# Performance work log

Measured on AMD Instinct MI355X. Metric: run time of the kernel, lower is better.

## Reference

```python
import jax, jax.numpy as jnp
import numpy as np

B, L, D, H, DK, DV = 16, 512, 1024, 16, 64, 64
EPS = 1e-3  # LayerNormalization eps (added to sigma, not variance)


def _xavier(key, shape):
    fan_in, fan_out = shape[-2], shape[-1]
    std = float(np.sqrt(2.0 / (fan_in + fan_out)))
    return jax.random.normal(key, shape, jnp.float32) * std


def setup_inputs() -> dict:
    key = jax.random.key(0)
    ks = jax.random.split(key, 8)
    q = jax.random.normal(ks[0], (B, L, D), jnp.float32)
    k = jax.random.normal(ks[1], (B, L, D), jnp.float32)
    v = jax.random.normal(ks[2], (B, L, D), jnp.float32)
    # key-padding mask: last 64 key positions masked (True => -inf)
    key_pad = jnp.arange(L) >= (L - 64)
    attn_mask = jnp.broadcast_to(key_pad[None, None, :], (B, L, L))
    w_qs = _xavier(ks[3], (H, D, DK))
    w_ks = _xavier(ks[4], (H, D, DK))
    w_vs = _xavier(ks[5], (H, D, DV))
    proj_w = _xavier(ks[6], (H * DV, D))  # stored as (in, out)
    proj_b = jnp.zeros((D,), jnp.float32)
    ln_a = jnp.ones((D,), jnp.float32)
    ln_b = jnp.zeros((D,), jnp.float32)
    return {"q": q, "k": k, "v": v, "attn_mask": attn_mask,
            "w_qs": w_qs, "w_ks": w_ks, "w_vs": w_vs,
            "proj_w": proj_w, "proj_b": proj_b, "ln_a": ln_a, "ln_b": ln_b}


def reference(q, k, v, attn_mask, w_qs, w_ks, w_vs, proj_w, proj_b, ln_a, ln_b):
    n_head, d_model = w_qs.shape[0], q.shape[-1]
    mb, len_q = q.shape[0], q.shape[1]
    temper = jnp.sqrt(jnp.asarray(d_model, q.dtype))  # NOTE: sqrt(d_model), not sqrt(d_k)
    residual = q
    # per-head projections: equivalent to repeat + bmm with (H, D, dk)
    q_s = jnp.einsum('bld,hdk->hblk', q, w_qs)   # [H,B,Lq,dk]
    k_s = jnp.einsum('bld,hdk->hblk', k, w_ks)   # [H,B,Lk,dk]
    v_s = jnp.einsum('bld,hdv->hblv', v, w_vs)   # [H,B,Lk,dv]
    attn = jnp.einsum('hbqd,hbkd->hbqk', q_s, k_s) / temper  # [H,B,Lq,Lk]
    attn = jnp.where(attn_mask[None], -jnp.inf, attn)
    attn = jax.nn.softmax(attn, axis=-1)
    # dropout is identity in eval mode
    ctx = jnp.einsum('hbqk,hbkv->hbqv', attn, v_s)  # [H,B,Lq,dv]
    # torch.cat(torch.split(outputs, mb, 0), -1): heads concatenated on last dim
    concat = jnp.transpose(ctx, (1, 2, 0, 3)).reshape(mb, len_q, n_head * ctx.shape[-1])
    out = concat @ proj_w + proj_b
    z = out + residual
    mu = jnp.mean(z, axis=-1, keepdims=True)
    sigma = jnp.std(z, axis=-1, keepdims=True, ddof=1)  # torch.std is unbiased
    ln = (z - mu) / (sigma + EPS) * ln_a + ln_b
    attns = attn.reshape(n_head * mb, len_q, attn.shape[-1])
    return ln, attns
```

## Files before the change

kernel.cpp:

```cpp
#include <hip/hip_runtime.h>
#include <math.h>

constexpr int Bc   = 16;
constexpr int Lc   = 512;
constexpr int Dc   = 1024;
constexpr int Hc   = 16;
constexpr int DKc  = 64;
constexpr int ROWS = Bc * Lc;
constexpr int MASK_START = Lc - 64;
constexpr int NKEY = MASK_START;
constexpr int NFS  = NKEY / 16;
constexpr int NKS  = NKEY / 32;
constexpr float TEMPER_INV = 1.0f / 32.0f;
constexpr float LN_EPS = 1e-3f;
constexpr size_t LN_ELEMS = (size_t)ROWS * Dc;
constexpr int PSTR = 456;

using u16 = unsigned short;
typedef __attribute__((ext_vector_type(8))) short bf16x8;
typedef __attribute__((ext_vector_type(4))) float f32x4;

__device__ __forceinline__ u16 f2bf(float f) {
    unsigned u = __float_as_uint(f);
    return (u16)((u + 0x7FFFu + ((u >> 16) & 1u)) >> 16);
}

__device__ __forceinline__ void gload16(const u16* g, u16* l) {
    __builtin_amdgcn_global_load_lds(
        (const __attribute__((address_space(1))) unsigned int*)g,
        (__attribute__((address_space(3))) unsigned int*)l, 16, 0, 0);
}

__global__ __launch_bounds__(256) void k_prep(
    const float* __restrict__ q, const float* __restrict__ k, const float* __restrict__ v,
    const float* __restrict__ wq, const float* __restrict__ wk, const float* __restrict__ wv,
    const float* __restrict__ pw,
    u16* __restrict__ qb, u16* __restrict__ kb, u16* __restrict__ vb,
    u16* __restrict__ wtq, u16* __restrict__ wtk, u16* __restrict__ wtv,
    u16* __restrict__ wto)
{
    const int bx = blockIdx.x;
    const int tid = threadIdx.x;
    __shared__ float t[32][33];

    if (bx < 24576) {
        const int z = bx >> 13;
        const int bxx = bx & 8191;
        const float* a = z == 0 ? q : (z == 1 ? k : v);
        u16* o = z == 0 ? qb : (z == 1 ? kb : vb);
        const size_t i = (size_t)bxx * 256 + tid;
        float4 x = ((const float4*)a)[i];
        ushort4 u;
        u.x = f2bf(x.x); u.y = f2bf(x.y); u.z = f2bf(x.z); u.w = f2bf(x.w);
        ((ushort4*)o)[i] = u;
    } else if (bx < 27648) {
        const int j = bx - 24576;
        const int z48 = j >> 6, rem = j & 63;
        const int gx = rem & 31, gy = rem >> 5;
        const int which = z48 >> 4, h = z48 & 15;
        const float* W = which == 0 ? wq : (which == 1 ? wk : wv);
        u16* O = which == 0 ? wtq : (which == 1 ? wtk : wtv);
        const int d0 = gx * 32, c0 = gy * 32;
        const int tx = tid & 31, ty = tid >> 5;
        #pragma unroll
        for (int i = 0; i < 4; ++i)
            t[ty + i*8][tx] = W[(size_t)h * (Dc*DKc) + (size_t)(d0 + ty + i*8) * DKc + c0 + tx];
        __syncthreads();
        #pragma unroll
        for (int i = 0; i < 4; ++i)
            O[(size_t)(h*64 + c0 + ty + i*8) * Dc + d0 + tx] = f2bf(t[tx][ty + i*8]);
    } else {
        const int j = bx - 27648;
        const int gx = j & 31, gy = j >> 5;
        const int d0 = gx * 32, n0 = gy * 32;
        const int tx = tid & 31, ty = tid >> 5;
        #pragma unroll
        for (int i = 0; i < 4; ++i)
            t[ty + i*8][tx] = pw[(size_t)(d0 + ty + i*8) * Dc + n0 + tx];
        __syncthreads();
        #pragma unroll
        for (int i = 0; i < 4; ++i)
            wto[(size_t)(n0 + ty + i*8) * Dc + d0 + tx] = f2bf(t[tx][ty + i*8]);
    }
}

__global__ __launch_bounds__(256) void k_gemm0(
    const u16* __restrict__ qb, const u16* __restrict__ kb, const u16* __restrict__ vb,
    const u16* __restrict__ wtq, const u16* __restrict__ wtk, const u16* __restrict__ wtv,
    u16* __restrict__ qc, u16* __restrict__ kc, u16* __restrict__ vt)
{
    const int z = blockIdx.z;
    const u16* A  = z == 0 ? qb : (z == 1 ? kb : vb);
    const u16* Bt = z == 0 ? wtq : (z == 1 ? wtk : wtv);

    const int tid  = threadIdx.x;
    const int wave = tid >> 6;
    const int lane = tid & 63;
    const int m0 = blockIdx.x * 128;
    const int n0 = blockIdx.y * 128;
    const int wm = (wave >> 1) * 64;
    const int wn = (wave & 1) * 64;

    __shared__ u16 As[2 * 128 * 32];
    __shared__ u16 Bs[2 * 128 * 32];

    f32x4 acc[4][4];
    #pragma unroll
    for (int mi = 0; mi < 4; ++mi)
        #pragma unroll
        for (int ni = 0; ni < 4; ++ni)
            acc[mi][ni] = f32x4{0.f, 0.f, 0.f, 0.f};

    const int grow = lane >> 2;
    const int gcol = (lane & 3) * 8;

    for (int k0 = 0; k0 < Dc; k0 += 64) {
        #pragma unroll
        for (int ii = 0; ii < 4; ++ii) {
            const int i = wave * 4 + ii;
            const int s = i >> 3;
            const int i7 = i & 7;
            const int r = i7 * 16 + grow;
            gload16(A  + (size_t)(m0 + r) * Dc + k0 + s*32 + gcol, &As[s*4096 + i7*512]);
            gload16(Bt + (size_t)(n0 + r) * Dc + k0 + s*32 + gcol, &Bs[s*4096 + i7*512]);
        }
        __syncthreads();
        #pragma unroll
        for (int s = 0; s < 2; ++s) {
            bf16x8 af[4], bfr[4];
            #pragma unroll
            for (int mi = 0; mi < 4; ++mi)
                af[mi] = *(const bf16x8*)&As[s*4096 + (wm + mi*16 + (lane & 15)) * 32 + (lane >> 4) * 8];
            #pragma unroll
            for (int ni = 0; ni < 4; ++ni)
                bfr[ni] = *(const bf16x8*)&Bs[s*4096 + (wn + ni*16 + (lane & 15)) * 32 + (lane >> 4) * 8];
            #pragma unroll
            for (int mi = 0; mi < 4; ++mi)
                #pragma unroll
                for (int ni = 0; ni < 4; ++ni)
                    acc[mi][ni] = __builtin_amdgcn_mfma_f32_16x16x32_bf16(af[mi], bfr[ni], acc[mi][ni], 0, 0, 0);
        }
        __syncthreads();
    }

    const int lc = lane & 15, lg = lane >> 4;
    if (z < 2) {
        u16* OB = z == 0 ? qc : kc;
        #pragma unroll
        for (int mi = 0; mi < 4; ++mi) {
            #pragma unroll
            for (int ni = 0; ni < 4; ++ni) {
                const int n = n0 + wn + ni*16 + lc;
                #pragma unroll
                for (int r = 0; r < 4; ++r) {
                    const int m = m0 + wm + mi*16 + lg*4 + r;
                    OB[(size_t)m * Dc + n] = f2bf(acc[mi][ni][r]);
                }
            }
        }
    } else {
        #pragma unroll
        for (int mi = 0; mi < 4; ++mi) {
            const int mbase = m0 + wm + mi*16 + lg*4;
            const int b  = mbase >> 9;
            const int kk = mbase & 511;
            #pragma unroll
            for (int ni = 0; ni < 4; ++ni) {
                const int n = n0 + wn + ni*16 + lc;
                const int h = n >> 6, d = n & 63;
                ushort4 o;
                o.x = f2bf(acc[mi][ni][0]); o.y = f2bf(acc[mi][ni][1]);
                o.z = f2bf(acc[mi][ni][2]); o.w = f2bf(acc[mi][ni][3]);
                *(ushort4*)&vt[((size_t)((h*16 + b)*64 + d)) * Lc + kk] = o;
            }
        }
    }
}

__global__ __launch_bounds__(256) void k_gemm1(
    const u16* __restrict__ A, const u16* __restrict__ Bt,
    float* __restrict__ OutF, const float* __restrict__ pb, const float* __restrict__ resid)
{
    const int tid  = threadIdx.x;
    const int wave = tid >> 6;
    const int lane = tid & 63;
    const int m0 = blockIdx.x * 128;
    const int n0 = blockIdx.y * 128;
    const int wm = (wave >> 1) * 64;
    const int wn = (wave & 1) * 64;

    __shared__ u16 As[2 * 128 * 32];
    __shared__ u16 Bs[2 * 128 * 32];

    f32x4 acc[4][4];
    #pragma unroll
    for (int mi = 0; mi < 4; ++mi)
        #pragma unroll
        for (int ni = 0; ni < 4; ++ni)
            acc[mi][ni] = f32x4{0.f, 0.f, 0.f, 0.f};

    const int grow = lane >> 2;
    const int gcol = (lane & 3) * 8;

    for (int k0 = 0; k0 < Dc; k0 += 64) {
        #pragma unroll
        for (int ii = 0; ii < 4; ++ii) {
            const int i = wave * 4 + ii;
            const int s = i >> 3;
            const int i7 = i & 7;
            const int r = i7 * 16 + grow;
            gload16(A  + (size_t)(m0 + r) * Dc + k0 + s*32 + gcol, &As[s*4096 + i7*512]);
            gload16(Bt + (size_t)(n0 + r) * Dc + k0 + s*32 + gcol, &Bs[s*4096 + i7*512]);
        }
        __syncthreads();
        #pragma unroll
        for (int s = 0; s < 2; ++s) {
            bf16x8 af[4], bfr[4];
            #pragma unroll
            for (int mi = 0; mi < 4; ++mi)
                af[mi] = *(const bf16x8*)&As[s*4096 + (wm + mi*16 + (lane & 15)) * 32 + (lane >> 4) * 8];
            #pragma unroll
            for (int ni = 0; ni < 4; ++ni)
                bfr[ni] = *(const bf16x8*)&Bs[s*4096 + (wn + ni*16 + (lane & 15)) * 32 + (lane >> 4) * 8];
            #pragma unroll
            for (int mi = 0; mi < 4; ++mi)
                #pragma unroll
                for (int ni = 0; ni < 4; ++ni)
                    acc[mi][ni] = __builtin_amdgcn_mfma_f32_16x16x32_bf16(af[mi], bfr[ni], acc[mi][ni], 0, 0, 0);
        }
        __syncthreads();
    }

    const int lc = lane & 15, lg = lane >> 4;
    #pragma unroll
    for (int mi = 0; mi < 4; ++mi) {
        #pragma unroll
        for (int ni = 0; ni < 4; ++ni) {
            const int n = n0 + wn + ni*16 + lc;
            #pragma unroll
            for (int r = 0; r < 4; ++r) {
                const int m = m0 + wm + mi*16 + lg*4 + r;
                OutF[(size_t)m * Dc + n] = acc[mi][ni][r] + pb[n] + resid[(size_t)m * Dc + n];
            }
        }
    }
}

__global__ __launch_bounds__(256, 2) void k_attn(
    const u16* __restrict__ qc, const u16* __restrict__ kc, const u16* __restrict__ vt,
    float* __restrict__ attn, u16* __restrict__ cc)
{
    const int hb = blockIdx.y;
    const int h = hb >> 4, b = hb & 15;
    const int q0 = blockIdx.x * 64;
    const int tid  = threadIdx.x;
    const int wave = tid >> 6;
    const int lane = tid & 63;
    const int wm = wave * 16;
    const int lc = lane & 15;
    const int lg = lane >> 4;

    __shared__ __align__(16) u16 pl[64 * PSTR];

    bf16x8 qa[2];
    {
        const size_t rowg = (size_t)(b*Lc + q0 + wm + lc) * Dc + h*64;
        qa[0] = *(const bf16x8*)&qc[rowg + 0*32 + lg*8];
        qa[1] = *(const bf16x8*)&qc[rowg + 1*32 + lg*8];
    }

    f32x4 s[NFS];
    #pragma unroll
    for (int nj = 0; nj < NFS; ++nj) {
        const size_t krow = (size_t)(b*Lc + nj*16 + lc) * Dc + h*64;
        bf16x8 kf0 = *(const bf16x8*)&kc[krow + 0*32 + lg*8];
        bf16x8 kf1 = *(const bf16x8*)&kc[krow + 1*32 + lg*8];
        f32x4 a = f32x4{0.f, 0.f, 0.f, 0.f};
        a = __builtin_amdgcn_mfma_f32_16x16x32_bf16(qa[0], kf0, a, 0, 0, 0);
        a = __builtin_amdgcn_mfma_f32_16x16x32_bf16(qa[1], kf1, a, 0, 0, 0);
        s[nj] = a;
    }

    float mx[4], sm[4];
    #pragma unroll
    for (int r = 0; r < 4; ++r) {
        float m = s[0][r];
        #pragma unroll
        for (int nj = 1; nj < NFS; ++nj) m = fmaxf(m, s[nj][r]);
        #pragma unroll
        for (int d = 1; d < 16; d <<= 1) m = fmaxf(m, __shfl_xor(m, d));
        mx[r] = m;
    }
    #pragma unroll
    for (int r = 0; r < 4; ++r) {
        float acc = 0.f;
        #pragma unroll
        for (int nj = 0; nj < NFS; ++nj) {
            float p = __expf((s[nj][r] - mx[r]) * TEMPER_INV);
            s[nj][r] = p;
            acc += p;
        }
        #pragma unroll
        for (int d = 1; d < 16; d <<= 1) acc += __shfl_xor(acc, d);
        sm[r] = 1.0f / acc;
    }

    float* S = attn + (size_t)hb * Lc * Lc;
    #pragma unroll
    for (int nj = 0; nj < NFS; ++nj) {
        #pragma unroll
        for (int r = 0; r < 4; ++r) {
            const int row = q0 + wm + lg*4 + r;
            const float p = s[nj][r] * sm[r];
            S[(size_t)row * Lc + nj*16 + lc] = p;
            pl[(wm + lg*4 + r) * PSTR + nj*16 + lc] = f2bf(p);
        }
    }
    {
        const float4 z4 = make_float4(0.f, 0.f, 0.f, 0.f);
        const int zr = q0 + wm + (lane >> 2);
        #pragma unroll
        for (int j = 0; j < 4; ++j)
            *(float4*)&S[(size_t)zr * Lc + MASK_START + ((lane & 3) + j*4) * 4] = z4;
    }

    const u16* Vt = vt + (size_t)hb * (64 * Lc);
    f32x4 o[4];
    #pragma unroll
    for (int ni = 0; ni < 4; ++ni) o[ni] = f32x4{0.f, 0.f, 0.f, 0.f};
    #pragma unroll
    for (int ks = 0; ks < NKS; ++ks) {
        bf16x8 pa = *(const bf16x8*)&pl[(wm + lc) * PSTR + ks*32 + lg*8];
        #pragma unroll
        for (int ni = 0; ni < 4; ++ni) {
            bf16x8 vb = *(const bf16x8*)&Vt[(size_t)(ni*16 + lc) * Lc + ks*32 + lg*8];
            o[ni] = __builtin_amdgcn_mfma_f32_16x16x32_bf16(pa, vb, o[ni], 0, 0, 0);
        }
    }
    #pragma unroll
    for (int ni = 0; ni < 4; ++ni) {
        #pragma unroll
        for (int r = 0; r < 4; ++r) {
            const int row = q0 + wm + lg*4 + r;
            cc[(size_t)(b*Lc + row) * Dc + h*64 + ni*16 + lc] = f2bf(o[ni][r]);
        }
    }
}

__global__ __launch_bounds__(256) void k_ln(
    float* __restrict__ z, const float* __restrict__ ga, const float* __restrict__ gb)
{
    const size_t row = blockIdx.x;
    float* p = z + row * Dc;
    const int tid = threadIdx.x;
    float4 x = ((const float4*)p)[tid];
    __shared__ float red[256];
    red[tid] = x.x + x.y + x.z + x.w; __syncthreads();
    for (int s = 128; s > 0; s >>= 1) { if (tid < s) red[tid] += red[tid + s]; __syncthreads(); }
    float mu = red[0] * (1.0f / Dc); __syncthreads();
    float dx = x.x - mu, dy = x.y - mu, dz = x.z - mu, dw = x.w - mu;
    red[tid] = dx*dx + dy*dy + dz*dz + dw*dw; __syncthreads();
    for (int s = 128; s > 0; s >>= 1) { if (tid < s) red[tid] += red[tid + s]; __syncthreads(); }
    float var = red[0] * (1.0f / (Dc - 1));
    float inv = 1.0f / (sqrtf(var) + LN_EPS);
    float4 a4 = ((const float4*)ga)[tid];
    float4 b4 = ((const float4*)gb)[tid];
    float4 o;
    o.x = dx * inv * a4.x + b4.x;
    o.y = dy * inv * a4.y + b4.y;
    o.z = dz * inv * a4.z + b4.z;
    o.w = dw * inv * a4.w + b4.w;
    ((float4*)p)[tid] = o;
}

extern "C" void kernel_launch(void* const* d_in, const int* in_sizes, int n_in,
                              void* d_out, int out_size, void* d_ws, size_t ws_size,
                              hipStream_t stream)
{
    const float* q  = (const float*)d_in[0];
    const float* k  = (const float*)d_in[1];
    const float* v  = (const float*)d_in[2];
    const float* wq = (const float*)d_in[4];
    const float* wk = (const float*)d_in[5];
    const float* wv = (const float*)d_in[6];
    const float* pw = (const float*)d_in[7];
    const float* pb = (const float*)d_in[8];
    const float* ga = (const float*)d_in[9];
    const float* gb = (const float*)d_in[10];

    float* ln_out   = (float*)d_out;
    float* attn_out = ln_out + LN_ELEMS;

    u16* qb  = (u16*)d_ws;
    u16* kb  = qb  + LN_ELEMS;
    u16* vb  = kb  + LN_ELEMS;
    u16* wtq = vb  + LN_ELEMS;
    u16* wtk = wtq + (size_t)Dc * Dc;
    u16* wtv = wtk + (size_t)Dc * Dc;
    u16* wto = wtv + (size_t)Dc * Dc;
    u16* qc  = wto + (size_t)Dc * Dc;
    u16* kc  = qc  + LN_ELEMS;
    u16* cc  = kc  + LN_ELEMS;
    u16* vt  = cc  + LN_ELEMS;

    hipLaunchKernelGGL(k_prep,  dim3(28672), dim3(256), 0, stream,
                       q, k, v, wq, wk, wv, pw, qb, kb, vb, wtq, wtk, wtv, wto);
    hipLaunchKernelGGL(k_gemm0, dim3(ROWS/128, Dc/128, 3), dim3(256), 0, stream,
                       qb, kb, vb, wtq, wtk, wtv, qc, kc, vt);
    hipLaunchKernelGGL(k_attn,  dim3(Lc/64, Hc*Bc), dim3(256), 0, stream,
                       qc, kc, vt, attn_out, cc);
    hipLaunchKernelGGL(k_gemm1, dim3(ROWS/128, Dc/128), dim3(256), 0, stream,
                       cc, wto, ln_out, pb, q);
    hipLaunchKernelGGL(k_ln,    dim3(ROWS), dim3(256), 0, stream,
                       ln_out, ga, gb);
}
```

Before: 302.2 us.

## Double-buffer LDS tiles in projection GEMMs to overlap loads with MFMA

Both GEMM kernels now use two LDS buffers per operand and prefetch the next K-tile while running MFMA on the current one, replacing the load-sync-compute-sync loop. The aim is to hide global-to-LDS load latency behind matrix math. This doubles LDS use per block, which may reduce occupancy. The loop still ends with one barrier per iteration, and that barrier must cover the async prefetch before the buffer is read.

```diff
diff --git a/kernel.cpp b/kernel.cpp
--- a/kernel.cpp
+++ b/kernel.cpp
@@ -101,8 +101,8 @@
     const int wm = (wave >> 1) * 64;
     const int wn = (wave & 1) * 64;
 
-    __shared__ u16 As[2 * 128 * 32];
-    __shared__ u16 Bs[2 * 128 * 32];
+    __shared__ u16 As[2 * 2 * 128 * 32];
+    __shared__ u16 Bs[2 * 2 * 128 * 32];
 
     f32x4 acc[4][4];
     #pragma unroll
@@ -114,26 +114,35 @@
     const int grow = lane >> 2;
     const int gcol = (lane & 3) * 8;
 
-    for (int k0 = 0; k0 < Dc; k0 += 64) {
+    auto stage = [&](int k0, int buf) {
         #pragma unroll
         for (int ii = 0; ii < 4; ++ii) {
             const int i = wave * 4 + ii;
             const int s = i >> 3;
             const int i7 = i & 7;
             const int r = i7 * 16 + grow;
-            gload16(A  + (size_t)(m0 + r) * Dc + k0 + s*32 + gcol, &As[s*4096 + i7*512]);
-            gload16(Bt + (size_t)(n0 + r) * Dc + k0 + s*32 + gcol, &Bs[s*4096 + i7*512]);
-        }
-        __syncthreads();
+            gload16(A  + (size_t)(m0 + r) * Dc + k0 + s*32 + gcol, &As[buf*8192 + s*4096 + i7*512]);
+            gload16(Bt + (size_t)(n0 + r) * Dc + k0 + s*32 + gcol, &Bs[buf*8192 + s*4096 + i7*512]);
+        }
+    };
+
+    stage(0, 0);
+    __syncthreads();
+
+    constexpr int NT = Dc / 64;
+    #pragma unroll 2
+    for (int t = 0; t < NT; ++t) {
+        const int cur = t & 1;
+        if (t + 1 < NT) stage((t + 1) * 64, cur ^ 1);
         #pragma unroll
         for (int s = 0; s < 2; ++s) {
             bf16x8 af[4], bfr[4];
             #pragma unroll
             for (int mi = 0; mi < 4; ++mi)
-                af[mi] = *(const bf16x8*)&As[s*4096 + (wm + mi*16 + (lane & 15)) * 32 + (lane >> 4) * 8];
+                af[mi] = *(const bf16x8*)&As[cur*8192 + s*4096 + (wm + mi*16 + (lane & 15)) * 32 + (lane >> 4) * 8];
             #pragma unroll
             for (int ni = 0; ni < 4; ++ni)
-                bfr[ni] = *(const bf16x8*)&Bs[s*4096 + (wn + ni*16 + (lane & 15)) * 32 + (lane >> 4) * 8];
+                bfr[ni] = *(const bf16x8*)&Bs[cur*8192 + s*4096 + (wn + ni*16 + (lane & 15)) * 32 + (lane >> 4) * 8];
             #pragma unroll
             for (int mi = 0; mi < 4; ++mi)
                 #pragma unroll
@@ -189,8 +198,8 @@
     const int wm = (wave >> 1) * 64;
     const int wn = (wave & 1) * 64;
 
-    __shared__ u16 As[2 * 128 * 32];
-    __shared__ u16 Bs[2 * 128 * 32];
+    __shared__ u16 As[2 * 2 * 128 * 32];
+    __shared__ u16 Bs[2 * 2 * 128 * 32];
 
     f32x4 acc[4][4];
     #pragma unroll
@@ -202,26 +211,35 @@
     const int grow = lane >> 2;
     const int gcol = (lane & 3) * 8;
 
-    for (int k0 = 0; k0 < Dc; k0 += 64) {
+    auto stage = [&](int k0, int buf) {
         #pragma unroll
         for (int ii = 0; ii < 4; ++ii) {
             const int i = wave * 4 + ii;
             const int s = i >> 3;
             const int i7 = i & 7;
             const int r = i7 * 16 + grow;
-            gload16(A  + (size_t)(m0 + r) * Dc + k0 + s*32 + gcol, &As[s*4096 + i7*512]);
-            gload16(Bt + (size_t)(n0 + r) * Dc + k0 + s*32 + gcol, &Bs[s*4096 + i7*512]);
-        }
-        __syncthreads();
+            gload16(A  + (size_t)(m0 + r) * Dc + k0 + s*32 + gcol, &As[buf*8192 + s*4096 + i7*512]);
+            gload16(Bt + (size_t)(n0 + r) * Dc + k0 + s*32 + gcol, &Bs[buf*8192 + s*4096 + i7*512]);
+        }
+    };
+
+    stage(0, 0);
+    __syncthreads();
+
+    constexpr int NT = Dc / 64;
+    #pragma unroll 2
+    for (int t = 0; t < NT; ++t) {
+        const int cur = t & 1;
+        if (t + 1 < NT) stage((t + 1) * 64, cur ^ 1);
         #pragma unroll
         for (int s = 0; s < 2; ++s) {
             bf16x8 af[4], bfr[4];
             #pragma unroll
             for (int mi = 0; mi < 4; ++mi)
-                af[mi] = *(const bf16x8*)&As[s*4096 + (wm + mi*16 + (lane & 15)) * 32 + (lane >> 4) * 8];
+                af[mi] = *(const bf16x8*)&As[cur*8192 + s*4096 + (wm + mi*16 + (lane & 15)) * 32 + (lane >> 4) * 8];
             #pragma unroll
             for (int ni = 0; ni < 4; ++ni)
-                bfr[ni] = *(const bf16x8*)&Bs[s*4096 + (wn + ni*16 + (lane & 15)) * 32 + (lane >> 4) * 8];
+                bfr[ni] = *(const bf16x8*)&Bs[cur*8192 + s*4096 + (wn + ni*16 + (lane & 15)) * 32 + (lane >> 4) * 8];
             #pragma unroll
             for (int mi = 0; mi < 4; ++mi)
                 #pragma unroll
```

Measured after the change: 312.1 us. 1.03x slower.
